# Performance work log

Measured on AMD Instinct MI355X. Metric: run time of the kernel, lower is better.

Reference implementation:

```python
import jax, jax.numpy as jnp
import numpy as np

HEADS = 8
HID = 256
D = HID // HEADS
NEG_SLOPE = 0.2  # PyG leaky_relu negative_slope default in HANConv
NA, NPAP, CIN = 10000, 20000, 256
E = 256000
OUT = 16


def seg_softmax(scores, seg, num_segments):
    # scores: [E, H]; softmax over edges sharing the same dst segment id
    m = jax.ops.segment_max(scores, seg, num_segments=num_segments)
    m = jnp.where(jnp.isfinite(m), m, 0.0)
    e = jnp.exp(scores - m[seg])
    s = jax.ops.segment_sum(e, seg, num_segments=num_segments)
    return e / (s[seg] + 1e-16)


def han_edge(h_src, h_dst, att_src, att_dst, src, dst, num_dst):
    # h_src: [Ns, H, D]; att_*: [H, D]; src/dst: [E]
    a = (h_src * att_src).sum(-1)[src] + (h_dst * att_dst).sum(-1)[dst]  # [E, H]
    alpha = seg_softmax(jax.nn.leaky_relu(a, NEG_SLOPE), dst, num_dst)
    out = jax.ops.segment_sum(h_src[src] * alpha[..., None], dst, num_segments=num_dst)
    return jax.nn.relu(out.reshape(num_dst, HID))


def semantic_group(xs, q, k_W, k_b):
    out = jnp.stack(xs)                                            # [M, N, F]
    score = (jnp.tanh(out @ k_W + k_b) * q).sum(-1).mean(axis=1)   # [M]
    attn = jax.nn.softmax(score)                                   # softmax over metapaths
    return (out * attn[:, None, None]).sum(0)                      # [N, F]


def setup_inputs() -> dict:
    key = jax.random.key(0)
    ks = jax.random.split(key, 32)
    n = lambda i, shape, s: jax.random.normal(ks[i], shape, dtype=jnp.float32) * s
    ri = lambda i, hi: jax.random.randint(ks[i], (E,), 0, hi).astype(jnp.int64)
    w_scale = (1.0 / CIN) ** 0.5
    return {
        "x_author": n(0, (NA, CIN), 1.0),
        "x_paper": n(1, (NPAP, CIN), 1.0),
        "W_author": n(2, (CIN, HID), w_scale),
        "b_author": jnp.zeros((HID,), jnp.float32),
        "W_paper": n(3, (CIN, HID), w_scale),
        "b_paper": jnp.zeros((HID,), jnp.float32),
        "att_sw": n(4, (HEADS, D), 0.1),
        "att_dw": n(5, (HEADS, D), 0.1),
        "att_sc": n(6, (HEADS, D), 0.1),
        "att_dc": n(7, (HEADS, D), 0.1),
        "att_sr": n(8, (HEADS, D), 0.1),
        "att_dr": n(9, (HEADS, D), 0.1),
        "k_W": n(10, (HID, HID), (1.0 / HID) ** 0.5),
        "k_b": jnp.zeros((HID,), jnp.float32),
        "q": n(11, (HID,), 0.1),
        "lin_W": n(12, (HID, OUT), (1.0 / HID) ** 0.5),
        "lin_b": jnp.zeros((OUT,), jnp.float32),
        "ew_src": ri(13, NA), "ew_dst": ri(14, NPAP),
        "ec_src": ri(15, NPAP), "ec_dst": ri(16, NPAP),
        "er_src": ri(17, NPAP), "er_dst": ri(18, NA),
    }


def reference(x_author, x_paper, W_author, b_author, W_paper, b_paper,
              att_sw, att_dw, att_sc, att_dc, att_sr, att_dr,
              k_W, k_b, q, lin_W, lin_b,
              ew_src, ew_dst, ec_src, ec_dst, er_src, er_dst):
    # per-node-type projection -> [N, H, D]
    h_a = (x_author @ W_author + b_author).reshape(NA, HEADS, D)
    h_p = (x_paper @ W_paper + b_paper).reshape(NPAP, HEADS, D)
    # per-edge-type gather / attention / segment-softmax / scatter
    o_writes = han_edge(h_a, h_p, att_sw, att_dw, ew_src, ew_dst, NPAP)  # author->paper
    o_cites = han_edge(h_p, h_p, att_sc, att_dc, ec_src, ec_dst, NPAP)   # paper->paper
    o_rev = han_edge(h_p, h_a, att_sr, att_dr, er_src, er_dst, NA)       # paper->author
    # semantic-level attention over metapaths per dst node type
    paper_out = semantic_group([o_writes, o_cites], q, k_W, k_b)
    author_out = semantic_group([o_rev], q, k_W, k_b)
    # global_add_pool per node type (batch=None -> single graph) + shared linear
    pooled = jnp.stack([author_out.sum(0), paper_out.sum(0)])  # [2, HID]
    return pooled @ lin_W + lin_b                              # [2, OUT]
```

## Files before the change

### kernel.cpp

```cpp
#include <hip/hip_runtime.h>
#include <hip/hip_bf16.h>

#define HEADS 8
#define HID 256
#define NA 10000
#define NPAP 20000
#define NE 256000
#define N_SEG (2 * NPAP + NA)
#define TOTE (3 * NE)
#define NEG_SLOPE 0.2f

typedef __attribute__((ext_vector_type(8))) short bf16x8;
typedef __attribute__((ext_vector_type(4))) float f32x4;

__device__ __forceinline__ short f2bf(float x) {
    unsigned u = __float_as_uint(x);
    unsigned r = (u + 0x7fffu + ((u >> 16) & 1u)) >> 16;
    return (short)r;
}
__device__ __forceinline__ float bf2f(short s) {
    return __uint_as_float(((unsigned)(unsigned short)s) << 16);
}
__device__ __forceinline__ float bflo(unsigned u) { return __uint_as_float(u << 16); }
__device__ __forceinline__ float bfhi(unsigned u) { return __uint_as_float(u & 0xffff0000u); }

#define CONV_BLKS 7500
#define W_BLKS 48
#define DEG_BLKS 3000
__global__ __launch_bounds__(256) void prep(
    const float* __restrict__ x_a, short* __restrict__ xab,
    const float* __restrict__ x_p, short* __restrict__ xpb,
    const float* __restrict__ W_a, short* __restrict__ WaT,
    const float* __restrict__ W_p, short* __restrict__ WpT,
    const float* __restrict__ k_W, short* __restrict__ kWT,
    const int* __restrict__ ewd, const int* __restrict__ ecd, const int* __restrict__ erd,
    int* __restrict__ deg)
{
    __shared__ short T[64][65];
    int b = blockIdx.x;
    int t = threadIdx.x;
    if (b < CONV_BLKS) {
        int i = (b * 256 + t) * 4;
        const float* in; short* out;
        const int n0 = NA * HID;
        if (i < n0) { in = x_a; out = xab; }
        else { i -= n0; in = x_p; out = xpb; }
        float4 v = *reinterpret_cast<const float4*>(&in[i]);
        short4 o;
        o.x = f2bf(v.x); o.y = f2bf(v.y); o.z = f2bf(v.z); o.w = f2bf(v.w);
        *reinterpret_cast<short4*>(&out[i]) = o;
    } else if (b < CONV_BLKS + W_BLKS) {
        int idx = b - CONV_BLKS;
        int z = idx >> 4, rem = idx & 15;
        int k0 = (rem & 3) * 64, c0 = (rem >> 2) * 64;
        const float* W = z == 0 ? W_a : (z == 1 ? W_p : k_W);
        short* Wt      = z == 0 ? WaT : (z == 1 ? WpT : kWT);
        int rr = t >> 6, c = t & 63;
#pragma unroll
        for (int p = 0; p < 16; ++p) {
            int r = rr + p * 4;
            T[c][r] = f2bf(W[(size_t)(k0 + r) * 256 + c0 + c]);
        }
        __syncthreads();
#pragma unroll
        for (int p = 0; p < 16; ++p) {
            int cc = rr + p * 4;
            Wt[(size_t)(c0 + cc) * 256 + k0 + c] = T[cc][c];
        }
    } else {
        int e = (b - CONV_BLKS - W_BLKS) * 256 + t;
        if (e >= TOTE) return;
        int d;
        if (e < NE)          d = ewd[e];
        else if (e < 2 * NE) d = ecd[e - NE] + NPAP;
        else                 d = erd[e - 2 * NE] + 2 * NPAP;
        atomicAdd(&deg[d], 1);
    }
}

template <int EP>
__global__ __launch_bounds__(256) void gemm_dual(
    const short* __restrict__ A0, const short* __restrict__ Wt0, const float* __restrict__ b0,
    short* __restrict__ C0, float* __restrict__ sAcc0, int N0, int nb0,
    const short* __restrict__ A1, const short* __restrict__ Wt1, const float* __restrict__ b1,
    short* __restrict__ C1, float* __restrict__ sAcc1, int N1,
    const float* __restrict__ q)
{
    __shared__ short As[64][64];
    __shared__ short Ws[256][64];
    __shared__ float red[256];

    int bx = blockIdx.x;
    const short* A; const short* Wt; const float* bias; short* Cb; float* sAcc; int N, row0;
    if (bx < nb0) { A = A0; Wt = Wt0; bias = b0; Cb = C0; sAcc = sAcc0; N = N0; row0 = bx * 64; }
    else          { A = A1; Wt = Wt1; bias = b1; Cb = C1; sAcc = sAcc1; N = N1; row0 = (bx - nb0) * 64; }

    int tid = threadIdx.x;
    int w = tid >> 6, l = tid & 63;
    int lr = l & 15, lh = l >> 4;
    int swz = (l & 7) << 3;

    f32x4 acc[4][4] = {};

    for (int k0 = 0; k0 < 256; k0 += 64) {
#pragma unroll
        for (int i = 0; i < 2; ++i) {
            int lin = tid + i * 256;
            int r = lin >> 3, kc = (lin & 7) << 3;
            bf16x8 v = {};
            int gr = row0 + r;
            if (gr < N) v = *reinterpret_cast<const bf16x8*>(&A[(size_t)gr * 256 + k0 + kc]);
            *reinterpret_cast<bf16x8*>(&As[r][kc ^ ((r & 7) << 3)]) = v;
        }
#pragma unroll
        for (int i = 0; i < 8; ++i) {
            int lin = tid + i * 256;
            int c = lin >> 3, kc = (lin & 7) << 3;
            *reinterpret_cast<bf16x8*>(&Ws[c][kc ^ ((c & 7) << 3)]) =
                *reinterpret_cast<const bf16x8*>(&Wt[(size_t)c * 256 + k0 + kc]);
        }
        __syncthreads();
#pragma unroll
        for (int kk = 0; kk < 64; kk += 32) {
            int krow = (kk + lh * 8) ^ swz;
            bf16x8 af[4], bfr[4];
#pragma unroll
            for (int mi = 0; mi < 4; ++mi)
                af[mi] = *reinterpret_cast<bf16x8*>(&As[mi * 16 + lr][krow]);
#pragma unroll
            for (int ni = 0; ni < 4; ++ni)
                bfr[ni] = *reinterpret_cast<bf16x8*>(&Ws[w * 64 + ni * 16 + lr][krow]);
#pragma unroll
            for (int mi = 0; mi < 4; ++mi)
#pragma unroll
                for (int ni = 0; ni < 4; ++ni)
                    acc[mi][ni] = __builtin_amdgcn_mfma_f32_16x16x32_bf16(
                        af[mi], bfr[ni], acc[mi][ni], 0, 0, 0);
        }
        __syncthreads();
    }

    if (EP == 0) {
#pragma unroll
        for (int mi = 0; mi < 4; ++mi) {
            int rb = row0 + mi * 16 + lh * 4;
#pragma unroll
            for (int ni = 0; ni < 4; ++ni) {
                int c = w * 64 + ni * 16 + lr;
                float bc = bias[c];
#pragma unroll
                for (int j = 0; j < 4; ++j) {
                    if (rb + j < N) Cb[(size_t)(rb + j) * 256 + c] = f2bf(acc[mi][ni][j] + bc);
                }
            }
        }
    } else {
        float s = 0.f;
#pragma unroll
        for (int mi = 0; mi < 4; ++mi) {
            int rb = row0 + mi * 16 + lh * 4;
#pragma unroll
            for (int ni = 0; ni < 4; ++ni) {
                int c = w * 64 + ni * 16 + lr;
                float bc = bias[c], qc = q[c];
#pragma unroll
                for (int j = 0; j < 4; ++j) {
                    if (rb + j < N) s += tanhf(acc[mi][ni][j] + bc) * qc;
                }
            }
        }
        red[tid] = s;
        __syncthreads();
        for (int k = 128; k > 0; k >>= 1) {
            if (tid < k) red[tid] += red[tid + k];
            __syncthreads();
        }
        if (tid == 0) atomicAdd(sAcc, red[0]);
    }
}

#define FP8_BLKS 3750
__global__ __launch_bounds__(256) void node_att_all(
    const short* __restrict__ h_p, const short* __restrict__ h_a,
    const float* __restrict__ att_dw, const float* __restrict__ att_sc,
    const float* __restrict__ att_dc, const float* __restrict__ att_sr,
    const float* __restrict__ att_sw, const float* __restrict__ att_dr,
    float* __restrict__ a_dw, float* __restrict__ a_sc,
    float* __restrict__ a_dc, float* __restrict__ a_sr,
    float* __restrict__ a_sw, float* __restrict__ a_dr,
    const short* __restrict__ hcat, unsigned char* __restrict__ h8cat)
{
    int n = blockIdx.x;
    int t = threadIdx.x;
    if (n < NPAP) {
        float v = bf2f(h_p[(size_t)n * 256 + t]);
        float d0 = v * att_dw[t], d1 = v * att_sc[t], d2 = v * att_dc[t], d3 = v * att_sr[t];
#pragma unroll
        for (int k = 16; k > 0; k >>= 1) {
            d0 += __shfl_xor(d0, k, 64);
            d1 += __shfl_xor(d1, k, 64);
            d2 += __shfl_xor(d2, k, 64);
            d3 += __shfl_xor(d3, k, 64);
        }
        if ((t & 31) == 0) {
            int hh = t >> 5;
            a_dw[n * 8 + hh] = d0; a_sc[n * 8 + hh] = d1;
            a_dc[n * 8 + hh] = d2; a_sr[n * 8 + hh] = d3;
        }
    } else if (n < NPAP + NA) {
        int m = n - NPAP;
        float v = bf2f(h_a[(size_t)m * 256 + t]);
        float d0 = v * att_sw[t], d1 = v * att_dr[t];
#pragma unroll
        for (int k = 16; k > 0; k >>= 1) {
            d0 += __shfl_xor(d0, k, 64);
            d1 += __shfl_xor(d1, k, 64);
        }
        if ((t & 31) == 0) {
            int hh = t >> 5;
            a_sw[m * 8 + hh] = d0; a_dr[m * 8 + hh] = d1;
        }
    } else {
        int idx = ((n - NPAP - NA) * 256 + t) * 8;
        uint4 vv = *reinterpret_cast<const uint4*>(&hcat[idx]);
        float f0 = bflo(vv.x), f1 = bfhi(vv.x);
        float f2 = bflo(vv.y), f3 = bfhi(vv.y);
        float f4 = bflo(vv.z), f5 = bfhi(vv.z);
        float f6 = bflo(vv.w), f7 = bfhi(vv.w);
        int w0 = __builtin_amdgcn_cvt_pk_fp8_f32(f0, f1, 0, false);
        w0 = __builtin_amdgcn_cvt_pk_fp8_f32(f2, f3, w0, true);
        int w1 = __builtin_amdgcn_cvt_pk_fp8_f32(f4, f5, 0, false);
        w1 = __builtin_amdgcn_cvt_pk_fp8_f32(f6, f7, w1, true);
        *reinterpret_cast<uint2*>(&h8cat[idx]) = make_uint2((unsigned)w0, (unsigned)w1);
    }
}

__global__ void scan_l1(const int* __restrict__ deg, int* __restrict__ excl,
                        int* __restrict__ bsum, int N)
{
    __shared__ int buf[256];
    int t = threadIdx.x;
    int base = blockIdx.x * 256;
    int v = (base + t < N) ? deg[base + t] : 0;
    buf[t] = v;
    __syncthreads();
    for (int off = 1; off < 256; off <<= 1) {
        int add = (t >= off) ? buf[t - off] : 0;
        __syncthreads();
        buf[t] += add;
        __syncthreads();
    }
    if (base + t < N) excl[base + t] = buf[t] - v;
    if (t == 255) bsum[blockIdx.x] = buf[255];
}

__global__ void scan_l2(const int* __restrict__ bsum, int* __restrict__ boff, int nb)
{
    __shared__ int buf[256];
    int t = threadIdx.x;
    int v = (t < nb) ? bsum[t] : 0;
    buf[t] = v;
    __syncthreads();
    for (int off = 1; off < 256; off <<= 1) {
        int add = (t >= off) ? buf[t - off] : 0;
        __syncthreads();
        buf[t] += add;
        __syncthreads();
    }
    if (t < nb) boff[t] = buf[t] - v;
}

__global__ void scan_l3(const int* __restrict__ excl, const int* __restrict__ boff,
                        int* __restrict__ starts, int* __restrict__ cursor, int N)
{
    int i = blockIdx.x * 256 + threadIdx.x;
    if (i > N) return;
    int v = (i == N) ? TOTE : excl[i] + boff[i >> 8];
    starts[i] = v;
    if (i < N) cursor[i] = v;
}

__global__ void place_edges3(const int* __restrict__ ews, const int* __restrict__ ewd,
                             const int* __restrict__ ecs, const int* __restrict__ ecd,
                             const int* __restrict__ ers, const int* __restrict__ erd,
                             int* __restrict__ cursor, int* __restrict__ ssrc)
{
    int e = blockIdx.x * 256 + threadIdx.x;
    if (e >= TOTE) return;
    int s, d;
    if (e < NE)          { s = ews[e];          d = ewd[e]; }
    else if (e < 2 * NE) { s = ecs[e - NE];     d = ecd[e - NE] + NPAP; }
    else                 { s = ers[e - 2 * NE]; d = erd[e - 2 * NE] + 2 * NPAP; }
    int pos = atomicAdd(&cursor[d], 1);
    ssrc[pos] = s;
}

__global__ __launch_bounds__(256) void han_seg(
    const int* __restrict__ starts, const int* __restrict__ ssrc,
    const float* __restrict__ a_sw, const float* __restrict__ a_dw,
    const float* __restrict__ a_sc, const float* __restrict__ a_dc,
    const float* __restrict__ a_sr, const float* __restrict__ a_dr,
    const unsigned* __restrict__ h8_a, const unsigned* __restrict__ h8_p,
    short* __restrict__ outall)
{
    int w = threadIdx.x >> 6, lane = threadIdx.x & 63;
    int n = blockIdx.x * 4 + w;
    if (n >= N_SEG) return;

    const float* asrc; const float* adst; const unsigned* h8;
    int nloc;
    if (n < NPAP)          { nloc = n;            asrc = a_sw; adst = a_dw; h8 = h8_a; }
    else if (n < 2 * NPAP) { nloc = n - NPAP;     asrc = a_sc; adst = a_dc; h8 = h8_p; }
    else                   { nloc = n - 2 * NPAP; asrc = a_sr; adst = a_dr; h8 = h8_p; }

    int hh = lane >> 3;
    int c0 = lane << 2;
    float ad = adst[nloc * 8 + hh];

    int i = starts[n], end = starts[n + 1];
    float ac0 = 0.f, ac1 = 0.f, ac2 = 0.f, ac3 = 0.f, ps = 0.f;

    for (; i + 4 <= end; i += 4) {
        int s0 = __builtin_amdgcn_readfirstlane(ssrc[i]);
        int s1 = __builtin_amdgcn_readfirstlane(ssrc[i + 1]);
        int s2 = __builtin_amdgcn_readfirstlane(ssrc[i + 2]);
        int s3 = __builtin_amdgcn_readfirstlane(ssrc[i + 3]);
        float x0 = asrc[s0 * 8 + hh] + ad;
        float x1 = asrc[s1 * 8 + hh] + ad;
        float x2 = asrc[s2 * 8 + hh] + ad;
        float x3 = asrc[s3 * 8 + hh] + ad;
        unsigned v0 = h8[s0 * 64 + lane];
        unsigned v1 = h8[s1 * 64 + lane];
        unsigned v2 = h8[s2 * 64 + lane];
        unsigned v3 = h8[s3 * 64 + lane];
        x0 = x0 > 0.f ? x0 : NEG_SLOPE * x0;
        x1 = x1 > 0.f ? x1 : NEG_SLOPE * x1;
        x2 = x2 > 0.f ? x2 : NEG_SLOPE * x2;
        x3 = x3 > 0.f ? x3 : NEG_SLOPE * x3;
        float e0 = __expf(x0), e1 = __expf(x1), e2 = __expf(x2), e3 = __expf(x3);
        ps += (e0 + e1) + (e2 + e3);
        ac0 += e0 * __builtin_amdgcn_cvt_f32_fp8(v0, 0) + e1 * __builtin_amdgcn_cvt_f32_fp8(v1, 0)
             + e2 * __builtin_amdgcn_cvt_f32_fp8(v2, 0) + e3 * __builtin_amdgcn_cvt_f32_fp8(v3, 0);
        ac1 += e0 * __builtin_amdgcn_cvt_f32_fp8(v0, 1) + e1 * __builtin_amdgcn_cvt_f32_fp8(v1, 1)
             + e2 * __builtin_amdgcn_cvt_f32_fp8(v2, 1) + e3 * __builtin_amdgcn_cvt_f32_fp8(v3, 1);
        ac2 += e0 * __builtin_amdgcn_cvt_f32_fp8(v0, 2) + e1 * __builtin_amdgcn_cvt_f32_fp8(v1, 2)
             + e2 * __builtin_amdgcn_cvt_f32_fp8(v2, 2) + e3 * __builtin_amdgcn_cvt_f32_fp8(v3, 2);
        ac3 += e0 * __builtin_amdgcn_cvt_f32_fp8(v0, 3) + e1 * __builtin_amdgcn_cvt_f32_fp8(v1, 3)
             + e2 * __builtin_amdgcn_cvt_f32_fp8(v2, 3) + e3 * __builtin_amdgcn_cvt_f32_fp8(v3, 3);
    }
    for (; i < end; ++i) {
        int s0 = __builtin_amdgcn_readfirstlane(ssrc[i]);
        float x0 = asrc[s0 * 8 + hh] + ad;
        unsigned v0 = h8[s0 * 64 + lane];
        x0 = x0 > 0.f ? x0 : NEG_SLOPE * x0;
        float e0 = __expf(x0);
        ps += e0;
        ac0 += e0 * __builtin_amdgcn_cvt_f32_fp8(v0, 0);
        ac1 += e0 * __builtin_amdgcn_cvt_f32_fp8(v0, 1);
        ac2 += e0 * __builtin_amdgcn_cvt_f32_fp8(v0, 2);
        ac3 += e0 * __builtin_amdgcn_cvt_f32_fp8(v0, 3);
    }

    float inv = 1.0f / (ps + 1e-16f);
    float o0 = ac0 * inv, o1 = ac1 * inv, o2 = ac2 * inv, o3 = ac3 * inv;
    short4 o;
    o.x = f2bf(o0 > 0.f ? o0 : 0.f);
    o.y = f2bf(o1 > 0.f ? o1 : 0.f);
    o.z = f2bf(o2 > 0.f ? o2 : 0.f);
    o.w = f2bf(o3 > 0.f ? o3 : 0.f);
    *reinterpret_cast<short4*>(&outall[(size_t)n * 256 + c0]) = o;
}

__global__ void colsum3(const short* __restrict__ outall,
                        float* __restrict__ cw, float* __restrict__ cc,
                        float* __restrict__ cr)
{
    int t = threadIdx.x;
    int r0 = blockIdx.x * 32;
    int rend = r0 + 32 < N_SEG ? r0 + 32 : N_SEG;
    float s = 0.f;
    for (int r = r0; r < rend; ++r) s += bf2f(outall[(size_t)r * 256 + t]);
    float* cs = r0 < NPAP ? cw : (r0 < 2 * NPAP ? cc : cr);
    atomicAdd(&cs[t], s);
}

__global__ void finalize(const float* __restrict__ scoreAcc,
                         const float* __restrict__ colsum_w, const float* __restrict__ colsum_c,
                         const float* __restrict__ colsum_r,
                         const float* __restrict__ lin_W, const float* __restrict__ lin_b,
                         float* __restrict__ out)
{
    int t = threadIdx.x;
    if (t >= 32) return;
    float sw = scoreAcc[0] / (float)NPAP;
    float scs = scoreAcc[1] / (float)NPAP;
    float mx = fmaxf(sw, scs);
    float ew = expf(sw - mx), ec = expf(scs - mx);
    float aw = ew / (ew + ec), ac = ec / (ew + ec);
    int row = t >> 4, j = t & 15;
    float acc = lin_b[j];
    for (int c = 0; c < 256; ++c) {
        float p = (row == 0) ? colsum_r[c] : (aw * colsum_w[c] + ac * colsum_c[c]);
        acc += p * lin_W[c * 16 + j];
    }
    out[row * 16 + j] = acc;
}

extern "C" void kernel_launch(void* const* d_in, const int* in_sizes, int n_in,
                              void* d_out, int out_size, void* d_ws, size_t ws_size,
                              hipStream_t stream)
{
    const float* x_a   = (const float*)d_in[0];
    const float* x_p   = (const float*)d_in[1];
    const float* W_a   = (const float*)d_in[2];
    const float* b_a   = (const float*)d_in[3];
    const float* W_p   = (const float*)d_in[4];
    const float* b_p   = (const float*)d_in[5];
    const float* att_sw = (const float*)d_in[6];
    const float* att_dw = (const float*)d_in[7];
    const float* att_sc = (const float*)d_in[8];
    const float* att_dc = (const float*)d_in[9];
    const float* att_sr = (const float*)d_in[10];
    const float* att_dr = (const float*)d_in[11];
    const float* k_W   = (const float*)d_in[12];
    const float* k_b   = (const float*)d_in[13];
    const float* q     = (const float*)d_in[14];
    const float* lin_W = (const float*)d_in[15];
    const float* lin_b = (const float*)d_in[16];
    const int* ew_src = (const int*)d_in[17];
    const int* ew_dst = (const int*)d_in[18];
    const int* ec_src = (const int*)d_in[19];
    const int* ec_dst = (const int*)d_in[20];
    const int* er_src = (const int*)d_in[21];
    const int* er_dst = (const int*)d_in[22];

    float* ws = (float*)d_ws;
    size_t off = 0;
    auto align4 = [&]() { off = (off + 3) & ~(size_t)3; };

    short* h_a_bf = (short*)(ws + off); off += (size_t)NA * HID / 2;
    short* h_p_bf = (short*)(ws + off); off += (size_t)NPAP * HID / 2;
    unsigned char* h8_a = (unsigned char*)(ws + off); off += (size_t)NA * HID / 4;
    unsigned char* h8_p = (unsigned char*)(ws + off); off += (size_t)NPAP * HID / 4;
    short* xab  = (short*)(ws + off); off += (size_t)NA * HID / 2;
    short* xpb  = (short*)(ws + off); off += (size_t)NPAP * HID / 2;
    short* WaT  = (short*)(ws + off); off += 256 * 256 / 2;
    short* WpT  = (short*)(ws + off); off += 256 * 256 / 2;
    short* kWT  = (short*)(ws + off); off += 256 * 256 / 2;
    float* a_sw = ws + off; off += (size_t)NA * 8;
    float* a_dw = ws + off; off += (size_t)NPAP * 8;
    float* a_sc = ws + off; off += (size_t)NPAP * 8;
    float* a_dc = ws + off; off += (size_t)NPAP * 8;
    float* a_sr = ws + off; off += (size_t)NPAP * 8;
    float* a_dr = ws + off; off += (size_t)NA * 8;
    short* outall = (short*)(ws + off); off += (size_t)N_SEG * HID / 2;
    int* starts = (int*)(ws + off); off += N_SEG + 1; align4();
    int* cursor = (int*)(ws + off); off += N_SEG + 1; align4();
    int* sexcl  = (int*)(ws + off); off += N_SEG + 1; align4();
    int* sbsum  = (int*)(ws + off); off += 256;
    int* sboff  = (int*)(ws + off); off += 256;
    int* ssrc   = (int*)(ws + off); off += TOTE;
    size_t zero_start = off;
    int* deg        = (int*)(ws + off); off += N_SEG + 1; align4();
    float* colsum_w = ws + off; off += 256;
    float* colsum_c = ws + off; off += 256;
    float* colsum_r = ws + off; off += 256;
    float* score    = ws + off; off += 2;
    size_t zero_bytes = (off - zero_start) * sizeof(float);

    hipMemsetAsync(ws + zero_start, 0, zero_bytes, stream);

    prep<<<CONV_BLKS + W_BLKS + DEG_BLKS, 256, 0, stream>>>(
        x_a, xab, x_p, xpb, W_a, WaT, W_p, WpT, k_W, kWT,
        ew_dst, ec_dst, er_dst, deg);

    const int nbA = (NA + 63) / 64, nbP = (NPAP + 63) / 64;
    gemm_dual<0><<<nbA + nbP, 256, 0, stream>>>(
        xab, WaT, b_a, h_a_bf, nullptr, NA, nbA,
        xpb, WpT, b_p, h_p_bf, nullptr, NPAP, nullptr);

    node_att_all<<<NPAP + NA + FP8_BLKS, 256, 0, stream>>>(
        h_p_bf, h_a_bf, att_dw, att_sc, att_dc, att_sr, att_sw, att_dr,
        a_dw, a_sc, a_dc, a_sr, a_sw, a_dr, h_a_bf, h8_a);

    const int nbS = (N_SEG + 255) / 256;
    scan_l1<<<nbS, 256, 0, stream>>>(deg, sexcl, sbsum, N_SEG);
    scan_l2<<<1, 256, 0, stream>>>(sbsum, sboff, nbS);
    scan_l3<<<(N_SEG + 1 + 255) / 256, 256, 0, stream>>>(sexcl, sboff, starts, cursor, N_SEG);
    place_edges3<<<(TOTE + 255) / 256, 256, 0, stream>>>(ew_src, ew_dst, ec_src, ec_dst,
                                                         er_src, er_dst, cursor, ssrc);

    han_seg<<<(N_SEG + 3) / 4, 256, 0, stream>>>(starts, ssrc, a_sw, a_dw, a_sc, a_dc, a_sr, a_dr,
                                                 (const unsigned*)h8_a, (const unsigned*)h8_p,
                                                 outall);

    colsum3<<<(N_SEG + 31) / 32, 256, 0, stream>>>(outall, colsum_w, colsum_c, colsum_r);
    gemm_dual<1><<<2 * nbP, 256, 0, stream>>>(
        outall, kWT, k_b, nullptr, score + 0, NPAP, nbP,
        outall + (size_t)NPAP * HID, kWT, k_b, nullptr, score + 1, NPAP, q);

    finalize<<<1, 64, 0, stream>>>(score, colsum_w, colsum_c, colsum_r, lin_W, lin_b, (float*)d_out);
}
```

Measured before the change: 271.8 us.

## Fuse input bf16 conversion and fp8 packing into projection GEMM; split degree atomics

The projection GEMM now loads the fp32 node features directly and converts them to bf16 while filling shared memory. This removes the separate conversion pass and its intermediate buffers. The GEMM epilogue also writes the fp8 copy of the projected features, so node_att_all no longer needs extra blocks to re-read the bf16 output for packing. Degree counting now spreads atomics over four privatized count arrays, which scan_l1 sums, to reduce contention. The trade-offs are scattered single-byte fp8 stores, twice the global A-load bytes per GEMM tile, and a larger zeroed workspace.

```diff
diff --git a/kernel.cpp b/kernel.cpp
--- a/kernel.cpp
+++ b/kernel.cpp
@@ -24,34 +24,20 @@
 __device__ __forceinline__ float bflo(unsigned u) { return __uint_as_float(u << 16); }
 __device__ __forceinline__ float bfhi(unsigned u) { return __uint_as_float(u & 0xffff0000u); }
 
-#define CONV_BLKS 7500
 #define W_BLKS 48
 #define DEG_BLKS 3000
 __global__ __launch_bounds__(256) void prep(
-    const float* __restrict__ x_a, short* __restrict__ xab,
-    const float* __restrict__ x_p, short* __restrict__ xpb,
     const float* __restrict__ W_a, short* __restrict__ WaT,
     const float* __restrict__ W_p, short* __restrict__ WpT,
     const float* __restrict__ k_W, short* __restrict__ kWT,
     const int* __restrict__ ewd, const int* __restrict__ ecd, const int* __restrict__ erd,
-    int* __restrict__ deg)
+    int* __restrict__ deg4)
 {
     __shared__ short T[64][65];
     int b = blockIdx.x;
     int t = threadIdx.x;
-    if (b < CONV_BLKS) {
-        int i = (b * 256 + t) * 4;
-        const float* in; short* out;
-        const int n0 = NA * HID;
-        if (i < n0) { in = x_a; out = xab; }
-        else { i -= n0; in = x_p; out = xpb; }
-        float4 v = *reinterpret_cast<const float4*>(&in[i]);
-        short4 o;
-        o.x = f2bf(v.x); o.y = f2bf(v.y); o.z = f2bf(v.z); o.w = f2bf(v.w);
-        *reinterpret_cast<short4*>(&out[i]) = o;
-    } else if (b < CONV_BLKS + W_BLKS) {
-        int idx = b - CONV_BLKS;
-        int z = idx >> 4, rem = idx & 15;
+    if (b < W_BLKS) {
+        int z = b >> 4, rem = b & 15;
         int k0 = (rem & 3) * 64, c0 = (rem >> 2) * 64;
         const float* W = z == 0 ? W_a : (z == 1 ? W_p : k_W);
         short* Wt      = z == 0 ? WaT : (z == 1 ? WpT : kWT);
@@ -68,22 +54,102 @@
             Wt[(size_t)(c0 + cc) * 256 + k0 + c] = T[cc][c];
         }
     } else {
-        int e = (b - CONV_BLKS - W_BLKS) * 256 + t;
+        int bb = b - W_BLKS;
+        int e = bb * 256 + t;
         if (e >= TOTE) return;
         int d;
         if (e < NE)          d = ewd[e];
         else if (e < 2 * NE) d = ecd[e - NE] + NPAP;
         else                 d = erd[e - 2 * NE] + 2 * NPAP;
-        atomicAdd(&deg[d], 1);
-    }
-}
-
-template <int EP>
-__global__ __launch_bounds__(256) void gemm_dual(
-    const short* __restrict__ A0, const short* __restrict__ Wt0, const float* __restrict__ b0,
-    short* __restrict__ C0, float* __restrict__ sAcc0, int N0, int nb0,
-    const short* __restrict__ A1, const short* __restrict__ Wt1, const float* __restrict__ b1,
-    short* __restrict__ C1, float* __restrict__ sAcc1, int N1,
+        atomicAdd(&deg4[(bb & 3) * N_SEG + d], 1);
+    }
+}
+
+__global__ __launch_bounds__(256) void proj_gemm(
+    const float* __restrict__ A0, const short* __restrict__ Wt0, const float* __restrict__ b0,
+    short* __restrict__ C0, unsigned char* __restrict__ H80, int N0, int nb0,
+    const float* __restrict__ A1, const short* __restrict__ Wt1, const float* __restrict__ b1,
+    short* __restrict__ C1, unsigned char* __restrict__ H81, int N1)
+{
+    __shared__ short As[64][64];
+    __shared__ short Ws[256][64];
+
+    int bx = blockIdx.x;
+    const float* A; const short* Wt; const float* bias; short* Cb; unsigned char* H8; int N, row0;
+    if (bx < nb0) { A = A0; Wt = Wt0; bias = b0; Cb = C0; H8 = H80; N = N0; row0 = bx * 64; }
+    else          { A = A1; Wt = Wt1; bias = b1; Cb = C1; H8 = H81; N = N1; row0 = (bx - nb0) * 64; }
+
+    int tid = threadIdx.x;
+    int w = tid >> 6, l = tid & 63;
+    int lr = l & 15, lh = l >> 4;
+    int swz = (l & 7) << 3;
+
+    f32x4 acc[4][4] = {};
+
+    for (int k0 = 0; k0 < 256; k0 += 64) {
+#pragma unroll
+        for (int i = 0; i < 4; ++i) {
+            int lin = tid + i * 256;
+            int r = lin >> 4, fc = (lin & 15) << 2;
+            float4 v = make_float4(0.f, 0.f, 0.f, 0.f);
+            int gr = row0 + r;
+            if (gr < N) v = *reinterpret_cast<const float4*>(&A[(size_t)gr * 256 + k0 + fc]);
+            short4 o;
+            o.x = f2bf(v.x); o.y = f2bf(v.y); o.z = f2bf(v.z); o.w = f2bf(v.w);
+            *reinterpret_cast<short4*>(&As[r][fc ^ ((r & 7) << 3)]) = o;
+        }
+#pragma unroll
+        for (int i = 0; i < 8; ++i) {
+            int lin = tid + i * 256;
+            int c = lin >> 3, kc = (lin & 7) << 3;
+            *reinterpret_cast<bf16x8*>(&Ws[c][kc ^ ((c & 7) << 3)]) =
+                *reinterpret_cast<const bf16x8*>(&Wt[(size_t)c * 256 + k0 + kc]);
+        }
+        __syncthreads();
+#pragma unroll
+        for (int kk = 0; kk < 64; kk += 32) {
+            int krow = (kk + lh * 8) ^ swz;
+            bf16x8 af[4], bfr[4];
+#pragma unroll
+            for (int mi = 0; mi < 4; ++mi)
+                af[mi] = *reinterpret_cast<bf16x8*>(&As[mi * 16 + lr][krow]);
+#pragma unroll
+            for (int ni = 0; ni < 4; ++ni)
+                bfr[ni] = *reinterpret_cast<bf16x8*>(&Ws[w * 64 + ni * 16 + lr][krow]);
+#pragma unroll
+            for (int mi = 0; mi < 4; ++mi)
+#pragma unroll
+                for (int ni = 0; ni < 4; ++ni)
+                    acc[mi][ni] = __builtin_amdgcn_mfma_f32_16x16x32_bf16(
+                        af[mi], bfr[ni], acc[mi][ni], 0, 0, 0);
+        }
+        __syncthreads();
+    }
+
+#pragma unroll
+    for (int mi = 0; mi < 4; ++mi) {
+        int rb = row0 + mi * 16 + lh * 4;
+#pragma unroll
+        for (int ni = 0; ni < 4; ++ni) {
+            int c = w * 64 + ni * 16 + lr;
+            float bc = bias[c];
+#pragma unroll
+            for (int j = 0; j < 4; ++j) {
+                if (rb + j < N) {
+                    float v = acc[mi][ni][j] + bc;
+                    Cb[(size_t)(rb + j) * 256 + c] = f2bf(v);
+                    unsigned pk = __builtin_amdgcn_cvt_pk_fp8_f32(v, v, 0, false);
+                    H8[(size_t)(rb + j) * 256 + c] = (unsigned char)pk;
+                }
+            }
+        }
+    }
+}
+
+__global__ __launch_bounds__(256) void gemm_score(
+    const short* __restrict__ A0, const short* __restrict__ Wt, const float* __restrict__ kb,
+    float* __restrict__ sAcc0, int N0, int nb0,
+    const short* __restrict__ A1, float* __restrict__ sAcc1, int N1,
     const float* __restrict__ q)
 {
     __shared__ short As[64][64];
@@ -91,9 +157,9 @@
     __shared__ float red[256];
 
     int bx = blockIdx.x;
-    const short* A; const short* Wt; const float* bias; short* Cb; float* sAcc; int N, row0;
-    if (bx < nb0) { A = A0; Wt = Wt0; bias = b0; Cb = C0; sAcc = sAcc0; N = N0; row0 = bx * 64; }
-    else          { A = A1; Wt = Wt1; bias = b1; Cb = C1; sAcc = sAcc1; N = N1; row0 = (bx - nb0) * 64; }
+    const short* A; float* sAcc; int N, row0;
+    if (bx < nb0) { A = A0; sAcc = sAcc0; N = N0; row0 = bx * 64; }
+    else          { A = A1; sAcc = sAcc1; N = N1; row0 = (bx - nb0) * 64; }
 
     int tid = threadIdx.x;
     int w = tid >> 6, l = tid & 63;
@@ -140,46 +206,29 @@
         __syncthreads();
     }
 
-    if (EP == 0) {
-#pragma unroll
-        for (int mi = 0; mi < 4; ++mi) {
-            int rb = row0 + mi * 16 + lh * 4;
-#pragma unroll
-            for (int ni = 0; ni < 4; ++ni) {
-                int c = w * 64 + ni * 16 + lr;
-                float bc = bias[c];
-#pragma unroll
-                for (int j = 0; j < 4; ++j) {
-                    if (rb + j < N) Cb[(size_t)(rb + j) * 256 + c] = f2bf(acc[mi][ni][j] + bc);
-                }
+    float s = 0.f;
+#pragma unroll
+    for (int mi = 0; mi < 4; ++mi) {
+        int rb = row0 + mi * 16 + lh * 4;
+#pragma unroll
+        for (int ni = 0; ni < 4; ++ni) {
+            int c = w * 64 + ni * 16 + lr;
+            float bc = kb[c], qc = q[c];
+#pragma unroll
+            for (int j = 0; j < 4; ++j) {
+                if (rb + j < N) s += tanhf(acc[mi][ni][j] + bc) * qc;
             }
         }
-    } else {
-        float s = 0.f;
-#pragma unroll
-        for (int mi = 0; mi < 4; ++mi) {
-            int rb = row0 + mi * 16 + lh * 4;
-#pragma unroll
-            for (int ni = 0; ni < 4; ++ni) {
-                int c = w * 64 + ni * 16 + lr;
-                float bc = bias[c], qc = q[c];
-#pragma unroll
-                for (int j = 0; j < 4; ++j) {
-                    if (rb + j < N) s += tanhf(acc[mi][ni][j] + bc) * qc;
-                }
-            }
-        }
-        red[tid] = s;
-        __syncthreads();
-        for (int k = 128; k > 0; k >>= 1) {
-            if (tid < k) red[tid] += red[tid + k];
-            __syncthreads();
-        }
-        if (tid == 0) atomicAdd(sAcc, red[0]);
-    }
-}
-
-#define FP8_BLKS 3750
+    }
+    red[tid] = s;
+    __syncthreads();
+    for (int k = 128; k > 0; k >>= 1) {
+        if (tid < k) red[tid] += red[tid + k];
+        __syncthreads();
+    }
+    if (tid == 0) atomicAdd(sAcc, red[0]);
+}
+
 __global__ __launch_bounds__(256) void node_att_all(
     const short* __restrict__ h_p, const short* __restrict__ h_a,
     const float* __restrict__ att_dw, const float* __restrict__ att_sc,
@@ -187,8 +236,7 @@
     const float* __restrict__ att_sw, const float* __restrict__ att_dr,
     float* __restrict__ a_dw, float* __restrict__ a_sc,
     float* __restrict__ a_dc, float* __restrict__ a_sr,
-    float* __restrict__ a_sw, float* __restrict__ a_dr,
-    const short* __restrict__ hcat, unsigned char* __restrict__ h8cat)
+    float* __restrict__ a_sw, float* __restrict__ a_dr)
 {
     int n = blockIdx.x;
     int t = threadIdx.x;
@@ -207,7 +255,7 @@
             a_dw[n * 8 + hh] = d0; a_sc[n * 8 + hh] = d1;
             a_dc[n * 8 + hh] = d2; a_sr[n * 8 + hh] = d3;
         }
-    } else if (n < NPAP + NA) {
+    } else {
         int m = n - NPAP;
         float v = bf2f(h_a[(size_t)m * 256 + t]);
         float d0 = v * att_sw[t], d1 = v * att_dr[t];
@@ -220,28 +268,19 @@
             int hh = t >> 5;
             a_sw[m * 8 + hh] = d0; a_dr[m * 8 + hh] = d1;
         }
-    } else {
-        int idx = ((n - NPAP - NA) * 256 + t) * 8;
-        uint4 vv = *reinterpret_cast<const uint4*>(&hcat[idx]);
-        float f0 = bflo(vv.x), f1 = bfhi(vv.x);
-        float f2 = bflo(vv.y), f3 = bfhi(vv.y);
-        float f4 = bflo(vv.z), f5 = bfhi(vv.z);
-        float f6 = bflo(vv.w), f7 = bfhi(vv.w);
-        int w0 = __builtin_amdgcn_cvt_pk_fp8_f32(f0, f1, 0, false);
-        w0 = __builtin_amdgcn_cvt_pk_fp8_f32(f2, f3, w0, true);
-        int w1 = __builtin_amdgcn_cvt_pk_fp8_f32(f4, f5, 0, false);
-        w1 = __builtin_amdgcn_cvt_pk_fp8_f32(f6, f7, w1, true);
-        *reinterpret_cast<uint2*>(&h8cat[idx]) = make_uint2((unsigned)w0, (unsigned)w1);
-    }
-}
-
-__global__ void scan_l1(const int* __restrict__ deg, int* __restrict__ excl,
+    }
+}
+
+__global__ void scan_l1(const int* __restrict__ deg4, int* __restrict__ excl,
                         int* __restrict__ bsum, int N)
 {
     __shared__ int buf[256];
     int t = threadIdx.x;
     int base = blockIdx.x * 256;
-    int v = (base + t < N) ? deg[base + t] : 0;
+    int idx = base + t;
+    int v = 0;
+    if (idx < N)
+        v = deg4[idx] + deg4[N_SEG + idx] + deg4[2 * N_SEG + idx] + deg4[3 * N_SEG + idx];
     buf[t] = v;
     __syncthreads();
     for (int off = 1; off < 256; off <<= 1) {
@@ -250,7 +289,7 @@
         buf[t] += add;
         __syncthreads();
     }
-    if (base + t < N) excl[base + t] = buf[t] - v;
+    if (idx < N) excl[idx] = buf[t] - v;
     if (t == 255) bsum[blockIdx.x] = buf[255];
 }
 
@@ -442,8 +481,6 @@
     short* h_p_bf = (short*)(ws + off); off += (size_t)NPAP * HID / 2;
     unsigned char* h8_a = (unsigned char*)(ws + off); off += (size_t)NA * HID / 4;
     unsigned char* h8_p = (unsigned char*)(ws + off); off += (size_t)NPAP * HID / 4;
-    short* xab  = (short*)(ws + off); off += (size_t)NA * HID / 2;
-    short* xpb  = (short*)(ws + off); off += (size_t)NPAP * HID / 2;
     short* WaT  = (short*)(ws + off); off += 256 * 256 / 2;
     short* WpT  = (short*)(ws + off); off += 256 * 256 / 2;
     short* kWT  = (short*)(ws + off); off += 256 * 256 / 2;
@@ -461,7 +498,7 @@
     int* sboff  = (int*)(ws + off); off += 256;
     int* ssrc   = (int*)(ws + off); off += TOTE;
     size_t zero_start = off;
-    int* deg        = (int*)(ws + off); off += N_SEG + 1; align4();
+    int* deg4       = (int*)(ws + off); off += 4 * N_SEG; align4();
     float* colsum_w = ws + off; off += 256;
     float* colsum_c = ws + off; off += 256;
     float* colsum_r = ws + off; off += 256;
@@ -470,21 +507,20 @@
 
     hipMemsetAsync(ws + zero_start, 0, zero_bytes, stream);
 
-    prep<<<CONV_BLKS + W_BLKS + DEG_BLKS, 256, 0, stream>>>(
-        x_a, xab, x_p, xpb, W_a, WaT, W_p, WpT, k_W, kWT,
-        ew_dst, ec_dst, er_dst, deg);
+    prep<<<W_BLKS + DEG_BLKS, 256, 0, stream>>>(
+        W_a, WaT, W_p, WpT, k_W, kWT, ew_dst, ec_dst, er_dst, deg4);
 
     const int nbA = (NA + 63) / 64, nbP = (NPAP + 63) / 64;
-    gemm_dual<0><<<nbA + nbP, 256, 0, stream>>>(
-        xab, WaT, b_a, h_a_bf, nullptr, NA, nbA,
-        xpb, WpT, b_p, h_p_bf, nullptr, NPAP, nullptr);
-
-    node_att_all<<<NPAP + NA + FP8_BLKS, 256, 0, stream>>>(
+    proj_gemm<<<nbA + nbP, 256, 0, stream>>>(
+        x_a, WaT, b_a, h_a_bf, h8_a, NA, nbA,
+        x_p, WpT, b_p, h_p_bf, h8_p, NPAP);
+
+    node_att_all<<<NPAP + NA, 256, 0, stream>>>(
         h_p_bf, h_a_bf, att_dw, att_sc, att_dc, att_sr, att_sw, att_dr,
-        a_dw, a_sc, a_dc, a_sr, a_sw, a_dr, h_a_bf, h8_a);
+        a_dw, a_sc, a_dc, a_sr, a_sw, a_dr);
 
     const int nbS = (N_SEG + 255) / 256;
-    scan_l1<<<nbS, 256, 0, stream>>>(deg, sexcl, sbsum, N_SEG);
+    scan_l1<<<nbS, 256, 0, stream>>>(deg4, sexcl, sbsum, N_SEG);
     scan_l2<<<1, 256, 0, stream>>>(sbsum, sboff, nbS);
     scan_l3<<<(N_SEG + 1 + 255) / 256, 256, 0, stream>>>(sexcl, sboff, starts, cursor, N_SEG);
     place_edges3<<<(TOTE + 255) / 256, 256, 0, stream>>>(ew_src, ew_dst, ec_src, ec_dst,
@@ -495,9 +531,9 @@
                                                  outall);
 
     colsum3<<<(N_SEG + 31) / 32, 256, 0, stream>>>(outall, colsum_w, colsum_c, colsum_r);
-    gemm_dual<1><<<2 * nbP, 256, 0, stream>>>(
-        outall, kWT, k_b, nullptr, score + 0, NPAP, nbP,
-        outall + (size_t)NPAP * HID, kWT, k_b, nullptr, score + 1, NPAP, q);
+    gemm_score<<<2 * nbP, 256, 0, stream>>>(
+        outall, kWT, k_b, score + 0, NPAP, nbP,
+        outall + (size_t)NPAP * HID, score + 1, NPAP, q);
 
     finalize<<<1, 64, 0, stream>>>(score, colsum_w, colsum_c, colsum_r, lin_W, lin_b, (float*)d_out);
 }
```

New measurement: 266.1 us. 1.02x faster.
